# Performance work log

Hardware: AMD Instinct MI355X
Metric: run time of the kernel (lower is better)

The kernel has to match this reference:

```python
import jax, jax.numpy as jnp
from jax import lax
import numpy as np

B, T, F, H = 4096, 512, 8, 16  # batch, seq, n_features, hidden_dim


def _lstm(x, Wih, Whh, bih, bhh):
    """PyTorch-convention LSTM over batch-first x [B,T,in].
    Returns (h_T [B,H], outputs [B,T,H]). Gate order: i, f, g, o."""
    Bn = x.shape[0]
    Hn = Whh.shape[1]
    xs = jnp.swapaxes(x, 0, 1)                       # [T,B,in]
    x_proj = xs @ Wih.T + (bih + bhh)                # precompute input GEMM: [T,B,4H]

    def step(carry, xp):
        h, c = carry
        gates = xp + h @ Whh.T                       # [B,4H]
        i, f, g, o = jnp.split(gates, 4, axis=-1)
        i = jax.nn.sigmoid(i)
        f = jax.nn.sigmoid(f)
        g = jnp.tanh(g)
        o = jax.nn.sigmoid(o)
        c = f * c + i * g
        h = o * jnp.tanh(c)
        return (h, c), h

    h0 = jnp.zeros((Bn, Hn), x.dtype)
    (hT, _), hs = lax.scan(step, (h0, h0), x_proj)
    return hT, jnp.swapaxes(hs, 0, 1)                # [B,H], [B,T,H]


def setup_inputs() -> dict:
    key = jax.random.key(0)
    ks = jax.random.split(key, 11)
    s_e = 1.0 / np.sqrt(H)
    u = lambda k, shp: jax.random.uniform(k, shp, jnp.float32, -s_e, s_e)
    return {
        "x": jax.random.normal(ks[0], (B, T, F), jnp.float32),
        "enc_Wih": u(ks[1], (4 * H, F)),
        "enc_Whh": u(ks[2], (4 * H, H)),
        "enc_bih": u(ks[3], (4 * H,)),
        "enc_bhh": u(ks[4], (4 * H,)),
        "dec_Wih": u(ks[5], (4 * H, H)),
        "dec_Whh": u(ks[6], (4 * H, H)),
        "dec_bih": u(ks[7], (4 * H,)),
        "dec_bhh": u(ks[8], (4 * H,)),
        "out_W": u(ks[9], (F, H)),
        "out_b": u(ks[10], (F,)),
    }


def reference(x, enc_Wih, enc_Whh, enc_bih, enc_bhh,
              dec_Wih, dec_Whh, dec_bih, dec_bhh, out_W, out_b):
    # encoder: keep only final hidden state h_T
    hT, _ = _lstm(x, enc_Wih, enc_Whh, enc_bih, enc_bhh)   # [B,H]
    # repeat over time: h.squeeze(0).unsqueeze(1).repeat(1,T,1)
    repeated = jnp.broadcast_to(hT[:, None, :], (x.shape[0], x.shape[1], hT.shape[1]))
    _, decoded = _lstm(repeated, dec_Wih, dec_Whh, dec_bih, dec_bhh)  # [B,T,H]
    return decoded @ out_W.T + out_b                       # [B,T,F]
```

## Files before the change

kernel.cpp:

```cpp
#include <hip/hip_runtime.h>

#define B_ 4096
#define T_ 512
#define F_ 8
#define H_ 16

typedef float f32x2 __attribute__((ext_vector_type(2)));
typedef float f32x4v __attribute__((ext_vector_type(4)));

__device__ __forceinline__ f32x2 pkfma(f32x2 a, f32x2 b, f32x2 c) {
    return __builtin_elementwise_fma(a, b, c);
}
#define SV2(v, a, b) __builtin_shufflevector(v, v, a, b)

#define LOG2E 1.442695041f
#define N2LOG2E (-2.885390082f)

__device__ __forceinline__ float sigf(float x) {
    return __builtin_amdgcn_rcpf(1.0f + __builtin_amdgcn_exp2f(-LOG2E * x));
}
__device__ __forceinline__ float tanh_f(float x) {
    return __builtin_fmaf(2.0f,
        __builtin_amdgcn_rcpf(1.0f + __builtin_amdgcn_exp2f(N2LOG2E * x)), -1.0f);
}

__global__ __launch_bounds__(256, 1) void lstm_ae_kernel(
    const float* __restrict__ x,
    const float* __restrict__ eWih, const float* __restrict__ eWhh,
    const float* __restrict__ ebih, const float* __restrict__ ebhh,
    const float* __restrict__ dWih, const float* __restrict__ dWhh,
    const float* __restrict__ dbih, const float* __restrict__ dbhh,
    const float* __restrict__ oW,   const float* __restrict__ ob,
    float* __restrict__ out)
{
    const int tid = threadIdx.x;
    const int wv  = tid >> 6;
    const int l   = tid & 63;
    const int cw  = l >> 4;
    const int u   = l & 15;
    const int bw  = blockIdx.x * 16 + wv * 4;
    const int b   = bw + cw;

    __shared__ __align__(16) f32x2 hsh[4][40];
    __shared__ __align__(16) f32x2 xsh[4][4][33][4];

    const f32x2 zero2 = {0.0f, 0.0f};

    f32x2 wh[4][8], wi[4][4];
    float bias[4];
#pragma unroll
    for (int g = 0; g < 4; ++g) {
        const int r = g * 16 + u;
        const f32x2* phh = (const f32x2*)(eWhh + r * 16);
#pragma unroll
        for (int p = 0; p < 8; ++p) wh[g][p] = phh[p];
        const f32x2* pih = (const f32x2*)(eWih + r * 8);
#pragma unroll
        for (int p = 0; p < 4; ++p) wi[g][p] = pih[p];
        bias[g] = ebih[r] + ebhh[r];
    }

    float c = 0.0f;
    f32x2 hb[8];
#pragma unroll
    for (int p = 0; p < 8; ++p) hb[p] = zero2;

    float* hp = (float*)&hsh[wv][cw * 10];

    const int ps = l >> 1, phx = l & 1;
    f32x4v xr[4];
#pragma unroll
    for (int i = 0; i < 4; ++i)
        xr[i] = *(const f32x4v*)(x + ((size_t)(bw + i) * T_ + ps) * F_ + phx * 4);

    for (int c0 = 0; c0 < T_; c0 += 32) {
        __builtin_amdgcn_wave_barrier();
#pragma unroll
        for (int i = 0; i < 4; ++i)
            *(f32x4v*)&xsh[wv][i][ps][phx * 2] = xr[i];
        __builtin_amdgcn_wave_barrier();
        if (c0 + 32 < T_) {
#pragma unroll
            for (int i = 0; i < 4; ++i)
                xr[i] = *(const f32x4v*)(
                    x + ((size_t)(bw + i) * T_ + (c0 + 32 + ps)) * F_ + phx * 4);
        }
        for (int s = 0; s < 32; ++s) {
            f32x4v xq0 = *(const f32x4v*)&xsh[wv][cw][s][0];
            f32x4v xq1 = *(const f32x4v*)&xsh[wv][cw][s][2];
            f32x2 x0 = SV2(xq0, 0, 1), x1 = SV2(xq0, 2, 3);
            f32x2 x2 = SV2(xq1, 0, 1), x3 = SV2(xq1, 2, 3);

            f32x2 acc[4];
#pragma unroll
            for (int g = 0; g < 4; ++g) {
                f32x2 a = pkfma(wi[g][0], x0, f32x2{bias[g], 0.0f});
                a = pkfma(wi[g][1], x1, a);
                a = pkfma(wi[g][2], x2, a);
                a = pkfma(wi[g][3], x3, a);
#pragma unroll
                for (int p = 0; p < 8; ++p) a = pkfma(wh[g][p], hb[p], a);
                acc[g] = a;
            }
            const float gi = sigf(acc[0].x + acc[0].y);
            const float gf = sigf(acc[1].x + acc[1].y);
            const float gg = tanh_f(acc[2].x + acc[2].y);
            const float go = sigf(acc[3].x + acc[3].y);
            c = __builtin_fmaf(gf, c, gi * gg);
            const float ht = go * tanh_f(c);

            __builtin_amdgcn_wave_barrier();
            hp[u] = ht;
            __builtin_amdgcn_wave_barrier();
            f32x4v h0 = *(const f32x4v*)&hp[0];
            f32x4v h1 = *(const f32x4v*)&hp[4];
            f32x4v h2 = *(const f32x4v*)&hp[8];
            f32x4v h3 = *(const f32x4v*)&hp[12];
            hb[0] = SV2(h0, 0, 1); hb[1] = SV2(h0, 2, 3);
            hb[2] = SV2(h1, 0, 1); hb[3] = SV2(h1, 2, 3);
            hb[4] = SV2(h2, 0, 1); hb[5] = SV2(h2, 2, 3);
            hb[6] = SV2(h3, 0, 1); hb[7] = SV2(h3, 2, 3);
        }
    }

    f32x2 wd[4][8];
    float xp[4];
#pragma unroll
    for (int g = 0; g < 4; ++g) {
        const int r = g * 16 + u;
        const f32x2* pih = (const f32x2*)(dWih + r * 16);
        f32x2 a = zero2;
#pragma unroll
        for (int p = 0; p < 8; ++p) a = pkfma(pih[p], hb[p], a);
        xp[g] = dbih[r] + dbhh[r] + a.x + a.y;
        const f32x2* phh = (const f32x2*)(dWhh + r * 16);
#pragma unroll
        for (int p = 0; p < 8; ++p) wd[g][p] = phh[p];
    }
    f32x2 wo[8];
    {
        const f32x2* po = (const f32x2*)(oW + (u & 7) * 16);
#pragma unroll
        for (int p = 0; p < 8; ++p) wo[p] = po[p];
    }
    const float obv = ob[u & 7];
    const bool st = (u < 8);
    float* outp = out + (size_t)b * (T_ * F_);

    c = 0.0f;
#pragma unroll
    for (int p = 0; p < 8; ++p) hb[p] = zero2;

    for (int t = 0; t < T_; ++t) {
        f32x2 acc[4];
#pragma unroll
        for (int g = 0; g < 4; ++g) {
            f32x2 a = pkfma(wd[g][0], hb[0], f32x2{xp[g], 0.0f});
#pragma unroll
            for (int p = 1; p < 8; ++p) a = pkfma(wd[g][p], hb[p], a);
            acc[g] = a;
        }
        const float gi = sigf(acc[0].x + acc[0].y);
        const float gf = sigf(acc[1].x + acc[1].y);
        const float gg = tanh_f(acc[2].x + acc[2].y);
        const float go = sigf(acc[3].x + acc[3].y);
        c = __builtin_fmaf(gf, c, gi * gg);
        const float ht = go * tanh_f(c);

        __builtin_amdgcn_wave_barrier();
        hp[u] = ht;
        __builtin_amdgcn_wave_barrier();
        f32x4v h0 = *(const f32x4v*)&hp[0];
        f32x4v h1 = *(const f32x4v*)&hp[4];
        f32x4v h2 = *(const f32x4v*)&hp[8];
        f32x4v h3 = *(const f32x4v*)&hp[12];
        hb[0] = SV2(h0, 0, 1); hb[1] = SV2(h0, 2, 3);
        hb[2] = SV2(h1, 0, 1); hb[3] = SV2(h1, 2, 3);
        hb[4] = SV2(h2, 0, 1); hb[5] = SV2(h2, 2, 3);
        hb[6] = SV2(h3, 0, 1); hb[7] = SV2(h3, 2, 3);

        f32x2 oa = pkfma(wo[0], hb[0], f32x2{obv, 0.0f});
#pragma unroll
        for (int p = 1; p < 8; ++p) oa = pkfma(wo[p], hb[p], oa);
        if (st) outp[t * F_ + u] = oa.x + oa.y;
    }
}

extern "C" void kernel_launch(void* const* d_in, const int* in_sizes, int n_in,
                              void* d_out, int out_size, void* d_ws, size_t ws_size,
                              hipStream_t stream) {
    (void)in_sizes; (void)n_in; (void)d_ws; (void)ws_size; (void)out_size;
    lstm_ae_kernel<<<dim3(B_ / 16), dim3(256), 0, stream>>>(
        (const float*)d_in[0],
        (const float*)d_in[1], (const float*)d_in[2],
        (const float*)d_in[3], (const float*)d_in[4],
        (const float*)d_in[5], (const float*)d_in[6],
        (const float*)d_in[7], (const float*)d_in[8],
        (const float*)d_in[9], (const float*)d_in[10],
        (float*)d_out);
}
```

Measured before the change: 353.9 us.

## Shorten LSTM recurrence critical path with split chains and fused gate math

Each encoder step now computes the next step's input projection after publishing h, so it sits off the recurrent dependency chain. Gate dot-products use two independent accumulator chains, and the hidden state ping-pongs between two register sets. The gate math folds sigmoid(i)*tanh(g) and sigmoid(o)*tanh(c) into single reciprocals, cutting transcendental ops per step. The decoder output projection for step t-1 runs after step t's h exchange, taking it off the latency path. The cost is extra registers, clamped tanh inputs, and slightly different rounding.

```diff
diff --git a/kernel.cpp b/kernel.cpp
--- a/kernel.cpp
+++ b/kernel.cpp
@@ -11,18 +11,10 @@
 __device__ __forceinline__ f32x2 pkfma(f32x2 a, f32x2 b, f32x2 c) {
     return __builtin_elementwise_fma(a, b, c);
 }
-#define SV2(v, a, b) __builtin_shufflevector(v, v, a, b)
-
-#define LOG2E 1.442695041f
-#define N2LOG2E (-2.885390082f)
-
-__device__ __forceinline__ float sigf(float x) {
-    return __builtin_amdgcn_rcpf(1.0f + __builtin_amdgcn_exp2f(-LOG2E * x));
-}
-__device__ __forceinline__ float tanh_f(float x) {
-    return __builtin_fmaf(2.0f,
-        __builtin_amdgcn_rcpf(1.0f + __builtin_amdgcn_exp2f(N2LOG2E * x)), -1.0f);
-}
+
+#define L2E 1.442695041f
+#define N2L2E (-2.885390082f)
+#define WB() __builtin_amdgcn_wave_barrier()
 
 __global__ __launch_bounds__(256, 1) void lstm_ae_kernel(
     const float* __restrict__ x,
@@ -46,8 +38,7 @@
 
     const f32x2 zero2 = {0.0f, 0.0f};
 
-    f32x2 wh[4][8], wi[4][4];
-    float bias[4];
+    f32x2 wh[4][8], wi[4][4], bias2[4];
 #pragma unroll
     for (int g = 0; g < 4; ++g) {
         const int r = g * 16 + u;
@@ -57,15 +48,16 @@
         const f32x2* pih = (const f32x2*)(eWih + r * 8);
 #pragma unroll
         for (int p = 0; p < 4; ++p) wi[g][p] = pih[p];
-        bias[g] = ebih[r] + ebhh[r];
+        bias2[g] = f32x2{ebih[r] + ebhh[r], 0.0f};
     }
 
     float c = 0.0f;
-    f32x2 hb[8];
-#pragma unroll
-    for (int p = 0; p < 8; ++p) hb[p] = zero2;
+    f32x2 hbA[8], hbB[8];
+#pragma unroll
+    for (int p = 0; p < 8; ++p) { hbA[p] = zero2; hbB[p] = zero2; }
 
     float* hp = (float*)&hsh[wv][cw * 10];
+    const f32x2* hv2 = (const f32x2*)hp;
 
     const int ps = l >> 1, phx = l & 1;
     f32x4v xr[4];
@@ -73,116 +65,161 @@
     for (int i = 0; i < 4; ++i)
         xr[i] = *(const f32x4v*)(x + ((size_t)(bw + i) * T_ + ps) * F_ + phx * 4);
 
+    f32x2 xaA[4], xaB[4];
+
+#define GATES()                                                           \
+    const float pi = __builtin_amdgcn_exp2f(-L2E * sg[0]);                \
+    const float pf = __builtin_amdgcn_exp2f(-L2E * sg[1]);                \
+    const float ug = __builtin_amdgcn_exp2f(N2L2E * fmaxf(sg[2], -30.f)); \
+    const float po = __builtin_amdgcn_exp2f(-L2E * sg[3]);                \
+    const float gf = __builtin_amdgcn_rcpf(1.0f + pf);                    \
+    const float ig = (1.0f - ug) *                                        \
+        __builtin_amdgcn_rcpf((1.0f + pi) * (1.0f + ug));                 \
+    c = __builtin_fmaf(gf, c, ig);                                        \
+    const float vc = __builtin_amdgcn_exp2f(N2L2E * fmaxf(c, -30.f));     \
+    const float ht = (1.0f - vc) *                                        \
+        __builtin_amdgcn_rcpf((1.0f + po) * (1.0f + vc));
+
+#define ENC_STEP(HIN, HOUT, S)                                            \
+    {                                                                     \
+         \
+        const f32x2* xrow = &xsh[wv][cw][(S) + 1][0];                     \
+        f32x2 q0 = xrow[0], q1 = xrow[1], q2 = xrow[2], q3 = xrow[3];     \
+        float sg[4];                                                      \
+        _Pragma("unroll")                                                 \
+        for (int g = 0; g < 4; ++g) {                                     \
+            f32x2 aa = xaA[g], ab = xaB[g];                               \
+            _Pragma("unroll")                                             \
+            for (int p = 0; p < 8; p += 2) {                              \
+                aa = pkfma(wh[g][p],   HIN[p],   aa);                     \
+                ab = pkfma(wh[g][p+1], HIN[p+1], ab);                     \
+            }                                                             \
+            f32x2 ts = aa + ab;                                           \
+            sg[g] = ts.x + ts.y;                                          \
+        }                                                                 \
+        GATES();                                                          \
+        WB();                                                             \
+        hp[u] = ht;                                                       \
+        WB();                                                             \
+        _Pragma("unroll")                                                 \
+        for (int p = 0; p < 8; ++p) HOUT[p] = hv2[p];    \
+        WB();                                                             \
+                          \
+        _Pragma("unroll")                                                 \
+        for (int g = 0; g < 4; ++g) {                                     \
+            f32x2 na = pkfma(wi[g][0], q0, bias2[g]);                     \
+            f32x2 nb = pkfma(wi[g][1], q1, zero2);                        \
+            xaA[g] = pkfma(wi[g][2], q2, na);                             \
+            xaB[g] = pkfma(wi[g][3], q3, nb);                             \
+        }                                                                 \
+    }
+
     for (int c0 = 0; c0 < T_; c0 += 32) {
-        __builtin_amdgcn_wave_barrier();
+        WB();
 #pragma unroll
         for (int i = 0; i < 4; ++i)
             *(f32x4v*)&xsh[wv][i][ps][phx * 2] = xr[i];
-        __builtin_amdgcn_wave_barrier();
+        WB();
         if (c0 + 32 < T_) {
 #pragma unroll
             for (int i = 0; i < 4; ++i)
                 xr[i] = *(const f32x4v*)(
                     x + ((size_t)(bw + i) * T_ + (c0 + 32 + ps)) * F_ + phx * 4);
         }
-        for (int s = 0; s < 32; ++s) {
-            f32x4v xq0 = *(const f32x4v*)&xsh[wv][cw][s][0];
-            f32x4v xq1 = *(const f32x4v*)&xsh[wv][cw][s][2];
-            f32x2 x0 = SV2(xq0, 0, 1), x1 = SV2(xq0, 2, 3);
-            f32x2 x2 = SV2(xq1, 0, 1), x3 = SV2(xq1, 2, 3);
-
-            f32x2 acc[4];
+        {
+            const f32x2* xrow = &xsh[wv][cw][0][0];
+            f32x2 x0 = xrow[0], x1 = xrow[1], x2 = xrow[2], x3 = xrow[3];
 #pragma unroll
             for (int g = 0; g < 4; ++g) {
-                f32x2 a = pkfma(wi[g][0], x0, f32x2{bias[g], 0.0f});
-                a = pkfma(wi[g][1], x1, a);
-                a = pkfma(wi[g][2], x2, a);
-                a = pkfma(wi[g][3], x3, a);
-#pragma unroll
-                for (int p = 0; p < 8; ++p) a = pkfma(wh[g][p], hb[p], a);
-                acc[g] = a;
+                f32x2 na = pkfma(wi[g][0], x0, bias2[g]);
+                f32x2 nb = pkfma(wi[g][1], x1, zero2);
+                xaA[g] = pkfma(wi[g][2], x2, na);
+                xaB[g] = pkfma(wi[g][3], x3, nb);
             }
-            const float gi = sigf(acc[0].x + acc[0].y);
-            const float gf = sigf(acc[1].x + acc[1].y);
-            const float gg = tanh_f(acc[2].x + acc[2].y);
-            const float go = sigf(acc[3].x + acc[3].y);
-            c = __builtin_fmaf(gf, c, gi * gg);
-            const float ht = go * tanh_f(c);
-
-            __builtin_amdgcn_wave_barrier();
-            hp[u] = ht;
-            __builtin_amdgcn_wave_barrier();
-            f32x4v h0 = *(const f32x4v*)&hp[0];
-            f32x4v h1 = *(const f32x4v*)&hp[4];
-            f32x4v h2 = *(const f32x4v*)&hp[8];
-            f32x4v h3 = *(const f32x4v*)&hp[12];
-            hb[0] = SV2(h0, 0, 1); hb[1] = SV2(h0, 2, 3);
-            hb[2] = SV2(h1, 0, 1); hb[3] = SV2(h1, 2, 3);
-            hb[4] = SV2(h2, 0, 1); hb[5] = SV2(h2, 2, 3);
-            hb[6] = SV2(h3, 0, 1); hb[7] = SV2(h3, 2, 3);
-        }
-    }
-
-    f32x2 wd[4][8];
-    float xp[4];
+        }
+        for (int s = 0; s < 32; s += 2) {
+            ENC_STEP(hbA, hbB, s);
+            ENC_STEP(hbB, hbA, s + 1);
+        }
+    }
+#undef ENC_STEP
+
+    f32x2 wd[4][8], xp2[4];
 #pragma unroll
     for (int g = 0; g < 4; ++g) {
         const int r = g * 16 + u;
         const f32x2* pih = (const f32x2*)(dWih + r * 16);
         f32x2 a = zero2;
 #pragma unroll
-        for (int p = 0; p < 8; ++p) a = pkfma(pih[p], hb[p], a);
-        xp[g] = dbih[r] + dbhh[r] + a.x + a.y;
+        for (int p = 0; p < 8; ++p) a = pkfma(pih[p], hbA[p], a);
+        xp2[g] = f32x2{dbih[r] + dbhh[r] + a.x + a.y, 0.0f};
         const f32x2* phh = (const f32x2*)(dWhh + r * 16);
 #pragma unroll
         for (int p = 0; p < 8; ++p) wd[g][p] = phh[p];
     }
     f32x2 wo[8];
     {
-        const f32x2* po = (const f32x2*)(oW + (u & 7) * 16);
-#pragma unroll
-        for (int p = 0; p < 8; ++p) wo[p] = po[p];
-    }
-    const float obv = ob[u & 7];
+        const f32x2* po2 = (const f32x2*)(oW + (u & 7) * 16);
+#pragma unroll
+        for (int p = 0; p < 8; ++p) wo[p] = po2[p];
+    }
+    const f32x2 ob2 = {ob[u & 7], 0.0f};
     const bool st = (u < 8);
     float* outp = out + (size_t)b * (T_ * F_);
 
     c = 0.0f;
 #pragma unroll
-    for (int p = 0; p < 8; ++p) hb[p] = zero2;
-
-    for (int t = 0; t < T_; ++t) {
-        f32x2 acc[4];
-#pragma unroll
-        for (int g = 0; g < 4; ++g) {
-            f32x2 a = pkfma(wd[g][0], hb[0], f32x2{xp[g], 0.0f});
-#pragma unroll
-            for (int p = 1; p < 8; ++p) a = pkfma(wd[g][p], hb[p], a);
-            acc[g] = a;
-        }
-        const float gi = sigf(acc[0].x + acc[0].y);
-        const float gf = sigf(acc[1].x + acc[1].y);
-        const float gg = tanh_f(acc[2].x + acc[2].y);
-        const float go = sigf(acc[3].x + acc[3].y);
-        c = __builtin_fmaf(gf, c, gi * gg);
-        const float ht = go * tanh_f(c);
-
-        __builtin_amdgcn_wave_barrier();
-        hp[u] = ht;
-        __builtin_amdgcn_wave_barrier();
-        f32x4v h0 = *(const f32x4v*)&hp[0];
-        f32x4v h1 = *(const f32x4v*)&hp[4];
-        f32x4v h2 = *(const f32x4v*)&hp[8];
-        f32x4v h3 = *(const f32x4v*)&hp[12];
-        hb[0] = SV2(h0, 0, 1); hb[1] = SV2(h0, 2, 3);
-        hb[2] = SV2(h1, 0, 1); hb[3] = SV2(h1, 2, 3);
-        hb[4] = SV2(h2, 0, 1); hb[5] = SV2(h2, 2, 3);
-        hb[6] = SV2(h3, 0, 1); hb[7] = SV2(h3, 2, 3);
-
-        f32x2 oa = pkfma(wo[0], hb[0], f32x2{obv, 0.0f});
-#pragma unroll
-        for (int p = 1; p < 8; ++p) oa = pkfma(wo[p], hb[p], oa);
-        if (st) outp[t * F_ + u] = oa.x + oa.y;
+    for (int p = 0; p < 8; ++p) { hbA[p] = zero2; hbB[p] = zero2; }
+
+#define DEC_STEP(HIN, HOUT, TT)                                           \
+    {                                                                     \
+        float sg[4];                                                      \
+        _Pragma("unroll")                                                 \
+        for (int g = 0; g < 4; ++g) {                                     \
+            f32x2 aa = pkfma(wd[g][0], HIN[0], xp2[g]);                   \
+            f32x2 ab = pkfma(wd[g][1], HIN[1], zero2);                    \
+            _Pragma("unroll")                                             \
+            for (int p = 2; p < 8; p += 2) {                              \
+                aa = pkfma(wd[g][p],   HIN[p],   aa);                     \
+                ab = pkfma(wd[g][p+1], HIN[p+1], ab);                     \
+            }                                                             \
+            f32x2 ts = aa + ab;                                           \
+            sg[g] = ts.x + ts.y;                                          \
+        }                                                                 \
+        GATES();                                                          \
+        WB();                                                             \
+        hp[u] = ht;                                                       \
+        WB();                                                             \
+        _Pragma("unroll")                                                 \
+        for (int p = 0; p < 8; ++p) HOUT[p] = hv2[p];    \
+        WB();                                                             \
+                  \
+        f32x2 oa  = pkfma(wo[0], HIN[0], ob2);                            \
+        f32x2 obb = pkfma(wo[1], HIN[1], zero2);                          \
+        _Pragma("unroll")                                                 \
+        for (int p = 2; p < 8; p += 2) {                                  \
+            oa  = pkfma(wo[p],   HIN[p],   oa);                           \
+            obb = pkfma(wo[p+1], HIN[p+1], obb);                          \
+        }                                                                 \
+        f32x2 to = oa + obb;                                              \
+        if (st && (TT) > 0) outp[((TT) - 1) * F_ + u] = to.x + to.y;      \
+    }
+
+    for (int t = 0; t < T_; t += 2) {
+        DEC_STEP(hbA, hbB, t);
+        DEC_STEP(hbB, hbA, t + 1);
+    }
+#undef DEC_STEP
+    {
+        f32x2 oa  = pkfma(wo[0], hbA[0], ob2);
+        f32x2 obb = pkfma(wo[1], hbA[1], zero2);
+#pragma unroll
+        for (int p = 2; p < 8; p += 2) {
+            oa  = pkfma(wo[p],   hbA[p],  oa);
+            obb = pkfma(wo[p+1], hbA[p+1], obb);
+        }
+        f32x2 to = oa + obb;
+        if (st) outp[(T_ - 1) * F_ + u] = to.x + to.y;
     }
 }
 
```

New measurement: 354.6 us. About the same (+0.2%).
